# Kernel tuning notes

Hardware: AMD Instinct MI355X
Metric: run time of the kernel (lower is better)

Reference implementation:

```python
import jax, jax.numpy as jnp
import numpy as np

BN_EPS = 1e-5
ITER_N = 5

def _bn(x, gamma, beta, mean, var, axis):
    shape = [1] * x.ndim
    shape[axis] = -1
    r = lambda v: v.reshape(shape)
    return (x - r(mean)) * (r(gamma) / jnp.sqrt(r(var) + BN_EPS)) + r(beta)

def _covpool(x):
    # x: (B, d, M); MPNCOV CovpoolLayer: y = x @ I_hat @ x^T, I_hat = (1/M)I - (1/M^2)11^T
    M = x.shape[-1]
    I_hat = (-1.0 / (M * M)) * jnp.ones((M, M), x.dtype) + (1.0 / M) * jnp.eye(M, dtype=x.dtype)
    return jnp.einsum('bdm,mn,ben->bde', x, I_hat, x)

def _sqrtm_ns(A, iterN=ITER_N):
    # MPNCOV SqrtmLayer: trace-normalized Newton-Schulz iteration
    d = A.shape[-1]
    I3 = 3.0 * jnp.eye(d, dtype=A.dtype)
    normA = jnp.trace(A, axis1=1, axis2=2) / 3.0          # (B,)
    A_n = A / normA[:, None, None]
    ZY = 0.5 * (I3 - A_n)
    Y = A_n @ ZY
    Z = ZY
    for _ in range(iterN - 2):
        ZY = 0.5 * (I3 - Z @ Y)
        Y = Y @ ZY
        Z = ZY @ Z
    YZY = 0.5 * (Y @ (I3 - Z @ Y))
    return YZY * jnp.sqrt(normA)[:, None, None]

def setup_inputs() -> dict:
    key = jax.random.key(0)
    ks = jax.random.split(key, 12)
    B, C, H, W = 64, 1024, 16, 16
    D, R = 128, H * W  # att_dim, sp_reso
    return {
        'x': jax.random.normal(ks[0], (B, C, H, W), jnp.float32),
        'w_dr': jax.random.normal(ks[1], (D, C), jnp.float32) * 0.02,
        'b_dr': jax.random.normal(ks[2], (D,), jnp.float32) * 0.02,
        'bn1_gamma': jnp.ones((D,), jnp.float32),
        'bn1_beta': jnp.zeros((D,), jnp.float32),
        'bn1_mean': jax.random.normal(ks[3], (D,), jnp.float32) * 0.1,
        'bn1_var': jax.random.uniform(ks[4], (D,), jnp.float32, 0.5, 1.5),
        'bn2_gamma': jnp.ones((R,), jnp.float32),
        'bn2_beta': jnp.zeros((R,), jnp.float32),
        'bn2_mean': jax.random.normal(ks[5], (R,), jnp.float32) * 0.1,
        'bn2_var': jax.random.uniform(ks[6], (R,), jnp.float32, 0.5, 1.5),
        'rc_w': jax.random.normal(ks[7], (R,), jnp.float32) * 0.1 + 1.0,
        'rc_b': jax.random.normal(ks[8], (R,), jnp.float32) * 0.02,
        'fc_w': jax.random.normal(ks[9], (R, R * R), jnp.float32) * 0.004,
        'fc_b': jax.random.normal(ks[10], (R,), jnp.float32) * 0.02,
    }

def reference(x, w_dr, b_dr, bn1_gamma, bn1_beta, bn1_mean, bn1_var,
              bn2_gamma, bn2_beta, bn2_mean, bn2_var, rc_w, rc_b, fc_w, fc_b):
    B, C, H, W = x.shape
    # 1x1 dimension-reduction conv + BN + ReLU
    y = jnp.einsum('bchw,dc->bdhw', x, w_dr) + b_dr[None, :, None, None]
    y = jax.nn.relu(_bn(y, bn1_gamma, bn1_beta, bn1_mean, bn1_var, axis=1))
    # (B, D, HW) -> (B, HW, D): HW spatial positions as 'channels', D as samples
    y = y.reshape(B, -1, H * W).transpose(0, 2, 1)
    cov = _covpool(y)                  # (B, HW, HW)
    s = _sqrtm_ns(cov, ITER_N)         # (B, HW, HW)
    # row BN over first HW axis (channels of the (B, HW, HW, 1) view)
    s = _bn(s, bn2_gamma, bn2_beta, bn2_mean, bn2_var, axis=1)
    # grouped (depthwise) 1x1 row conv: per-row scale + bias
    s = s * rc_w[None, :, None] + rc_b[None, :, None]
    att = jax.nn.sigmoid(s.reshape(B, -1) @ fc_w.T + fc_b)   # (B, HW)
    att = att.reshape(B, 1, H, W)
    return x * att
```

## Files before the change

### kernel.cpp

```cpp
#include <hip/hip_runtime.h>

typedef unsigned short u16;
typedef unsigned int   u32;
typedef __attribute__((ext_vector_type(8))) short bf8;
typedef __attribute__((ext_vector_type(4))) float f4;
typedef __attribute__((ext_vector_type(16))) float f16f;

#define MFMA(a,b,c)   __builtin_amdgcn_mfma_f32_16x16x32_bf16(a,b,c,0,0,0)
#define MFMA32(a,b,c) __builtin_amdgcn_mfma_f32_32x32x16_bf16(a,b,c,0,0,0)

__device__ __forceinline__ u16 f2bf(float f){
  u32 u = __float_as_uint(f);
  u += 0x7fffu + ((u >> 16) & 1u);
  return (u16)(u >> 16);
}
__device__ __forceinline__ float bf2f(u16 h){ return __uint_as_float(((u32)h) << 16); }
__device__ __forceinline__ u32 pk2(float a, float b){ return (u32)f2bf(a) | ((u32)f2bf(b) << 16); }

__device__ __forceinline__ void glds16(const u16* g, u16* l){
  __builtin_amdgcn_global_load_lds((const __attribute__((address_space(1))) u32*)g,
                                   (__attribute__((address_space(3))) u32*)l, 16, 0, 0);
}

__device__ __forceinline__ bf8 ldsFrag(const char* m, int row0, int k0, int pitch){
  int l = threadIdx.x & 63;
  int r = row0 + (l & 15);
  int kb = ((k0 + ((l >> 4) << 3)) << 1) ^ ((r & 7) << 4);
  return *(const bf8*)(m + r * pitch + kb);
}
__device__ __forceinline__ void ldsPut(char* m, int row, int col, int pitch, u16 v){
  int kb = (col << 1) ^ ((row & 7) << 4);
  *(u16*)(m + row * pitch + kb) = v;
}

__device__ __forceinline__ bf8 fragNS(const char* m, int r0, int ks, int l){
  int r = r0 + (l & 31);
  int kb = ((ks << 5) + ((l >> 5) << 4)) ^ ((r & 15) << 4);
  return *(const bf8*)(m + r * 256 + kb);
}
__device__ __forceinline__ bf8 fragWT(const char* m, int r0, int ks, int l){
  int r = r0 + (l & 31);
  int kb = ((ks << 5) + ((l >> 5) << 4)) ^ ((r & 15) << 4);
  return *(const bf8*)(m + r * 512 + kb);
}
__device__ __forceinline__ char* nsAddr(char* m, int row, int col4){
  return m + row * 256 + ((col4 << 1) ^ ((row & 15) << 4));
}

__device__ __forceinline__ void mmPass(const char* A, const char* B, f16f (&acc)[2][2],
                                       int R0, int C0, int l){
  #pragma unroll
  for (int ks = 0; ks < 8; ++ks){
    bf8 a0 = fragNS(A, R0,      ks, l);
    bf8 a1 = fragNS(A, R0 + 32, ks, l);
    bf8 b0 = fragNS(B, C0,      ks, l);
    bf8 b1 = fragNS(B, C0 + 32, ks, l);
    acc[0][0] = MFMA32(a0, b0, acc[0][0]); acc[0][1] = MFMA32(a0, b1, acc[0][1]);
    acc[1][0] = MFMA32(a1, b0, acc[1][0]); acc[1][1] = MFMA32(a1, b1, acc[1][1]);
  }
}

__device__ __forceinline__ void writeTile(char* D, const f16f (&acc)[2][2], int R0, int C0, int l,
                                          float scale, float dval, const uint2* adv){
  #pragma unroll
  for (int ri = 0; ri < 2; ++ri)
  #pragma unroll
  for (int ci = 0; ci < 2; ++ci)
  #pragma unroll
  for (int g = 0; g < 4; ++g){
    int srow = C0 + ci * 32 + (l & 31);
    int scol = R0 + ri * 32 + g * 8 + ((l >> 5) << 2);
    float v[4];
    #pragma unroll
    for (int q = 0; q < 4; ++q){
      float x = scale * acc[ri][ci][g * 4 + q];
      x += ((scol + q) == srow) ? dval : 0.f;
      v[q] = x;
    }
    if (adv){
      uint2 ad = adv[(ri * 2 + ci) * 4 + g];
      v[0] += 1.5f * bf2f((u16)ad.x);
      v[1] += 1.5f * bf2f((u16)(ad.x >> 16));
      v[2] += 1.5f * bf2f((u16)ad.y);
      v[3] += 1.5f * bf2f((u16)(ad.y >> 16));
    }
    *(uint2*)nsAddr(D, srow, scol) = make_uint2(pk2(v[0], v[1]), pk2(v[2], v[3]));
  }
}

__global__ __launch_bounds__(256) void k_prep(const float* __restrict__ wdr,
                                              float* __restrict__ logits,
                                              u16* __restrict__ prep){
  int i = blockIdx.x * 256 + threadIdx.x;
  if (i < 16384) logits[i] = 0.f;
  #pragma unroll
  for (int j = 0; j < 2; ++j){
    int e = i + j * 65536;
    int chunk = e >> 13, rem = e & 8191, d = rem >> 6, cb2 = rem & 63;
    int c = ((cb2 * 2) ^ ((d & 7) << 4)) >> 1;
    prep[e] = f2bf(wdr[d * 1024 + chunk * 64 + c]);
  }
}

__global__ __launch_bounds__(512) void k_conv(
    const u16* __restrict__ wprep, const float* __restrict__ x, const float* __restrict__ bdr,
    const float* __restrict__ g1, const float* __restrict__ be1,
    const float* __restrict__ m1, const float* __restrict__ v1,
    u16* __restrict__ Wg, u16* __restrict__ WTg){
  __shared__ union {
    struct { u16 A[2][8192]; u16 Bt[2][2048]; } s;
    struct { float y[128 * 33]; float musum[512]; float mu[32]; } e;
  } sm;
  int t = threadIdx.x;
  int b = blockIdx.x >> 3, hw0 = (blockIdx.x & 7) * 32;
  const float* xb = x + (size_t)b * 262144 + hw0;

  int w = t >> 6, l = t & 63;
  int d0 = (w >> 1) * 32, hh = (w & 1) * 16;
  int lc = l & 15, lr = (l >> 4) * 4;

  const f4 fz = {0.f, 0.f, 0.f, 0.f};
  f4 acc[2]; acc[0] = fz; acc[1] = fz;

  int cp = t >> 5, hwl = t & 31;
  int bo0 = (4 * cp) ^ ((hwl & 7) << 4);
  int bo1 = (4 * cp + 64) ^ ((hwl & 7) << 4);

  glds16(wprep + t * 8,        sm.s.A[0] + t * 8);
  glds16(wprep + 4096 + t * 8, sm.s.A[0] + 4096 + t * 8);
  glds16(wprep + 8192 + t * 8,        sm.s.A[1] + t * 8);
  glds16(wprep + 8192 + 4096 + t * 8, sm.s.A[1] + 4096 + t * 8);
  float br0 = xb[(size_t)(2 * cp)      * 256 + hwl];
  float br1 = xb[(size_t)(2 * cp + 1)  * 256 + hwl];
  float br2 = xb[(size_t)(2 * cp + 32) * 256 + hwl];
  float br3 = xb[(size_t)(2 * cp + 33) * 256 + hwl];

  #pragma unroll
  for (int k = 0; k < 16; ++k){
    if (k >= 1 && k < 15){
      const u16* src = wprep + (k + 1) * 8192;
      glds16(src + t * 8,        sm.s.A[(k + 1) & 1] + t * 8);
      glds16(src + 4096 + t * 8, sm.s.A[(k + 1) & 1] + 4096 + t * 8);
    }
    float nb0 = 0.f, nb1 = 0.f, nb2 = 0.f, nb3 = 0.f;
    if (k < 15){
      int c0 = (k + 1) * 64;
      nb0 = xb[(size_t)(c0 + 2 * cp)      * 256 + hwl];
      nb1 = xb[(size_t)(c0 + 2 * cp + 1)  * 256 + hwl];
      nb2 = xb[(size_t)(c0 + 2 * cp + 32) * 256 + hwl];
      nb3 = xb[(size_t)(c0 + 2 * cp + 33) * 256 + hwl];
    }
    __builtin_amdgcn_sched_barrier(0);
    if (k == 0)       asm volatile("s_waitcnt vmcnt(4)" ::: "memory");
    else if (k == 15) asm volatile("s_waitcnt vmcnt(0)" ::: "memory");
    else              asm volatile("s_waitcnt vmcnt(6)" ::: "memory");
    __builtin_amdgcn_sched_barrier(0);
    *(u32*)((char*)sm.s.Bt[k & 1] + hwl * 128 + bo0) = pk2(br0, br1);
    *(u32*)((char*)sm.s.Bt[k & 1] + hwl * 128 + bo1) = pk2(br2, br3);
    asm volatile("s_waitcnt lgkmcnt(0)" ::: "memory");
    __builtin_amdgcn_sched_barrier(0);
    __builtin_amdgcn_s_barrier();
    __builtin_amdgcn_sched_barrier(0);
    #pragma unroll
    for (int ks = 0; ks < 2; ++ks){
      int k0 = ks * 32;
      bf8 a0 = ldsFrag((const char*)sm.s.A[k & 1], d0,      k0, 128);
      bf8 a1 = ldsFrag((const char*)sm.s.A[k & 1], d0 + 16, k0, 128);
      bf8 b0 = ldsFrag((const char*)sm.s.Bt[k & 1], hh, k0, 128);
      acc[0] = MFMA(a0, b0, acc[0]);
      acc[1] = MFMA(a1, b0, acc[1]);
    }
    __builtin_amdgcn_sched_barrier(0);
    __builtin_amdgcn_s_barrier();
    __builtin_amdgcn_sched_barrier(0);
    br0 = nb0; br1 = nb1; br2 = nb2; br3 = nb3;
  }
  __syncthreads();

  #pragma unroll
  for (int i = 0; i < 2; ++i)
    #pragma unroll
    for (int r = 0; r < 4; ++r){
      int d = d0 + i * 16 + lr + r;
      float s1 = g1[d] * rsqrtf(v1[d] + 1e-5f);
      float t1 = (bdr[d] - m1[d]) * s1 + be1[d];
      int hwp = hh + lc;
      sm.e.y[d * 33 + hwp] = fmaxf(acc[i][r] * s1 + t1, 0.f);
    }
  __syncthreads();
  {
    int part = t >> 5, col = t & 31;
    float s = 0.f;
    #pragma unroll
    for (int i2 = 0; i2 < 8; ++i2) s += sm.e.y[(part * 8 + i2) * 33 + col];
    sm.e.musum[part * 32 + col] = s;
  }
  __syncthreads();
  if (t < 32){
    float m = 0.f;
    #pragma unroll
    for (int p = 0; p < 16; ++p) m += sm.e.musum[p * 32 + t];
    sm.e.mu[t] = m * (1.0f / 128.0f);
  }
  __syncthreads();
  const float ISM = 0.08838834764831845f;
  {
    int hwp = t >> 4, dc = (t & 15) * 8;
    float muv = sm.e.mu[hwp];
    u32 q[4];
    #pragma unroll
    for (int jj = 0; jj < 4; ++jj){
      float a = (sm.e.y[(dc + 2 * jj)     * 33 + hwp] - muv) * ISM;
      float c = (sm.e.y[(dc + 2 * jj + 1) * 33 + hwp] - muv) * ISM;
      q[jj] = pk2(a, c);
    }
    *(uint4*)(Wg + ((size_t)(b * 256 + hw0 + hwp) * 128 + dc)) = make_uint4(q[0], q[1], q[2], q[3]);
  }
  {
    int d = t >> 2, hc = (t & 3) * 8;
    u32 q[4];
    #pragma unroll
    for (int jj = 0; jj < 4; ++jj){
      int h0 = hc + 2 * jj, h1 = hc + 2 * jj + 1;
      float a = (sm.e.y[d * 33 + h0] - sm.e.mu[h0]) * ISM;
      float c = (sm.e.y[d * 33 + h1] - sm.e.mu[h1]) * ISM;
      q[jj] = pk2(a, c);
    }
    *(uint4*)(WTg + ((size_t)(b * 128 + d) * 256 + hw0 + hc)) = make_uint4(q[0], q[1], q[2], q[3]);
  }
}

extern __shared__ char smns[];
__global__ __launch_bounds__(512, 2) void k_ns(const u16* __restrict__ WT,
                                               u16* __restrict__ yf, float* __restrict__ normAg){
  int b = blockIdx.x, t = threadIdx.x;
  char* Yb = smns;
  char* Zb = smns + 32768;
  char* T1 = smns + 65536;
  char* T2 = smns + 98304;
  char* T3 = smns + 131072;
  char* WTl = smns + 65536;
  char* G   = T3;
  float* trp = (float*)smns;

  int w = t >> 6, l = t & 63;
  int wq = w & 3;
  int R0 = (wq >> 1) * 64, C0 = (wq & 1) * 64;

  { const u16* src = WT + (size_t)b * 32768;
    int row = t >> 2, q = t & 3;
    #pragma unroll
    for (int j = 0; j < 8; ++j) {
      int c16 = q + j * 4;
      bf8 v = *(const bf8*)(src + row * 256 + c16 * 8);
      int ph = c16 ^ (row & 15);
      *(bf8*)(WTl + row * 512 + ph * 16) = v;
    }
  }
  if (t == 0) *trp = 0.f;
  __syncthreads();

  int R0g = (w & 3) * 32, C0g = (w >> 2) * 64;
  const f16f fz16 = {};
  f16f gac[2]; gac[0] = fz16; gac[1] = fz16;
  #pragma unroll
  for (int ks = 0; ks < 16; ++ks){
    bf8 a  = fragWT(WTl, R0g,      ks, l);
    bf8 b0 = fragWT(WTl, C0g,      ks, l);
    bf8 b1 = fragWT(WTl, C0g + 32, ks, l);
    gac[0] = MFMA32(a, b0, gac[0]);
    gac[1] = MFMA32(a, b1, gac[1]);
  }
  float tp = 0.f;
  #pragma unroll
  for (int ci = 0; ci < 2; ++ci)
    #pragma unroll
    for (int e = 0; e < 16; ++e){
      int row = R0g + (e & 3) + 8 * (e >> 2) + ((l >> 5) << 2);
      int col = C0g + ci * 32 + (l & 31);
      if (row == col) tp += gac[ci][e];
    }
  #pragma unroll
  for (int off = 32; off > 0; off >>= 1) tp += __shfl_down(tp, off);
  if (l == 0) atomicAdd(trp, tp);
  __syncthreads();

  float normA = fmaxf(*trp / 3.0f, 1e-12f);
  if (t == 0) normAg[b] = normA;
  float inv = 1.0f / normA;
  #pragma unroll
  for (int ci = 0; ci < 2; ++ci)
    #pragma unroll
    for (int g = 0; g < 4; ++g){
      int srow = C0g + ci * 32 + (l & 31);
      int scol = R0g + g * 8 + ((l >> 5) << 2);
      float v0 = gac[ci][g * 4 + 0] * inv, v1 = gac[ci][g * 4 + 1] * inv;
      float v2 = gac[ci][g * 4 + 2] * inv, v3 = gac[ci][g * 4 + 3] * inv;
      *(uint2*)nsAddr(G, srow, scol) = make_uint2(pk2(v0, v1), pk2(v2, v3));
    }
  __syncthreads();

  bf8 gA[8], gB[8];
  #pragma unroll
  for (int ks = 0; ks < 8; ++ks){
    gA[ks] = fragNS(G, C0,      ks, l);
    gB[ks] = fragNS(G, C0 + 32, ks, l);
  }
  { int row = t >> 2, q4 = t & 3;
    #pragma unroll
    for (int j = 0; j < 4; ++j){
      int c16 = q4 * 4 + j;
      int ph = c16 ^ (row & 15);
      bf8 gg = *(const bf8*)(G + row * 256 + ph * 16);
      bf8 yv, zv;
      #pragma unroll
      for (int e = 0; e < 8; ++e){
        int col = c16 * 8 + e;
        float y = -0.5f * bf2f((u16)gg[e]) + ((col == row) ? 1.5f : 0.f);
        yv[e] = (short)f2bf(y);
        zv[e] = (col == row) ? (short)f2bf(-0.5f) : (short)0;
      }
      *(bf8*)(Yb + row * 256 + ph * 16) = yv;
      *(bf8*)(Zb + row * 256 + ph * 16) = zv;
    }
  }
  __syncthreads();

  float z0 = 1.5f;
  for (int it = 0; it < 4; ++it){
    {
      f16f acc[2][2]; acc[0][0] = fz16; acc[0][1] = fz16; acc[1][0] = fz16; acc[1][1] = fz16;
      const char* As = (w < 4) ? Zb : Yb;
      #pragma unroll
      for (int ks = 0; ks < 8; ++ks){
        bf8 a0 = fragNS(As, R0,      ks, l);
        bf8 a1 = fragNS(As, R0 + 32, ks, l);
        acc[0][0] = MFMA32(a0, gA[ks], acc[0][0]); acc[0][1] = MFMA32(a0, gB[ks], acc[0][1]);
        acc[1][0] = MFMA32(a1, gA[ks], acc[1][0]); acc[1][1] = MFMA32(a1, gB[ks], acc[1][1]);
      }
      writeTile((w < 4) ? T1 : T3, acc, R0, C0, l, 1.0f, (w < 4) ? z0 : 0.f, nullptr);
    }
    __syncthreads();

    uint2 adv[16];
    {
      const char* addsrc = (w < 4) ? Zb : Yb;
      #pragma unroll
      for (int ri = 0; ri < 2; ++ri)
      #pragma unroll
      for (int ci = 0; ci < 2; ++ci)
      #pragma unroll
      for (int g = 0; g < 4; ++g){
        int srow = C0 + ci * 32 + (l & 31);
        int scol = R0 + ri * 32 + g * 8 + ((l >> 5) << 2);
        adv[(ri * 2 + ci) * 4 + g] = *(const uint2*)nsAddr((char*)addsrc, srow, scol);
      }
      if (w < 4){
        f16f acc[2][2]; acc[0][0] = fz16; acc[0][1] = fz16; acc[1][0] = fz16; acc[1][1] = fz16;
        mmPass(T1, Yb, acc, R0, C0, l);
        writeTile(T2, acc, R0, C0, l, -0.5f, 0.f, nullptr);
      }
    }
    __syncthreads();

    if ((w >= 4) || (it < 3)){
      f16f acc[2][2]; acc[0][0] = fz16; acc[0][1] = fz16; acc[1][0] = fz16; acc[1][1] = fz16;
      const char* A3 = (w < 4) ? T2 : T3;
      const char* B3 = (w < 4) ? T1 : T2;
      mmPass(A3, B3, acc, R0, C0, l);
      writeTile((w < 4) ? Zb : Yb, acc, R0, C0, l, 1.0f, 0.f, adv);
    }
    __syncthreads();
    z0 *= 1.5f;
  }

  { int row = t >> 2, q = t & 3;
    u16* dst = yf + (size_t)b * 16384 + row * 128;
    #pragma unroll
    for (int j = 0; j < 4; ++j) {
      int c16 = q * 4 + j;
      int ph = c16 ^ (row & 15);
      *(bf8*)(dst + c16 * 8) = *(const bf8*)(Yb + row * 256 + ph * 16);
    }
  }
}

extern __shared__ char smex[];
__global__ __launch_bounds__(512) void k_expand(
    const u16* __restrict__ Wg, const u16* __restrict__ yf, const float* __restrict__ normAg,
    const float* __restrict__ g2, const float* __restrict__ be2, const float* __restrict__ m2,
    const float* __restrict__ v2, const float* __restrict__ rcw, const float* __restrict__ rcb,
    u16* __restrict__ sp){
  int blk = blockIdx.x, b = blk >> 2, iband = blk & 3;
  char* Bm = smex;
  char* Yl = smex + 65536;
  char* El = smex + 98304;
  int t = threadIdx.x;
  { const u16* src = Wg + (size_t)b * 32768;
    int row = t >> 1, q = t & 1;
    #pragma unroll
    for (int j = 0; j < 8; ++j) {
      int c16 = q + j * 2;
      bf8 v = *(const bf8*)(src + row * 128 + c16 * 8);
      int ph = c16 ^ (row & 7);
      *(bf8*)(Bm + row * 256 + ph * 16) = v;
    } }
  { const u16* src = yf + (size_t)b * 16384;
    int row = t >> 2, q = t & 3;
    #pragma unroll
    for (int j = 0; j < 4; ++j) {
      int c16 = q + j * 4;
      bf8 v = *(const bf8*)(src + row * 128 + c16 * 8);
      int ph = c16 ^ (row & 7);
      *(bf8*)(Yl + row * 256 + ph * 16) = v;
    } }
  __syncthreads();
  int w = t >> 6, l = t & 63, lc = l & 15, lr = (l >> 4) * 4;
  const f4 fz = {0.f, 0.f, 0.f, 0.f};
  { int r0 = (w >> 2) * 32, c0 = (w & 3) * 32;
    f4 acc[2][2];
    acc[0][0] = fz; acc[0][1] = fz; acc[1][0] = fz; acc[1][1] = fz;
    #pragma unroll
    for (int kk = 0; kk < 4; ++kk) {
      int k0 = kk * 32;
      bf8 a0 = ldsFrag(Bm, iband * 64 + r0,      k0, 256);
      bf8 a1 = ldsFrag(Bm, iband * 64 + r0 + 16, k0, 256);
      bf8 b0 = ldsFrag(Yl, c0,      k0, 256);
      bf8 b1 = ldsFrag(Yl, c0 + 16, k0, 256);
      acc[0][0] = MFMA(a0, b0, acc[0][0]); acc[0][1] = MFMA(a0, b1, acc[0][1]);
      acc[1][0] = MFMA(a1, b0, acc[1][0]); acc[1][1] = MFMA(a1, b1, acc[1][1]);
    }
    #pragma unroll
    for (int i = 0; i < 2; ++i)
      #pragma unroll
      for (int j = 0; j < 2; ++j)
        #pragma unroll
        for (int r = 0; r < 4; ++r)
          ldsPut(El, r0 + i * 16 + lr + r, c0 + j * 16 + lc, 256, f2bf(acc[i][j][r]));
  }
  __syncthreads();
  { float invs = rsqrtf(normAg[b]);
    int r0 = (w >> 2) * 32, c0 = (w & 3) * 64;
    f4 acc[2][4];
    #pragma unroll
    for (int i = 0; i < 2; ++i)
      #pragma unroll
      for (int j = 0; j < 4; ++j) acc[i][j] = fz;
    #pragma unroll
    for (int kk = 0; kk < 4; ++kk) {
      int k0 = kk * 32;
      bf8 a0 = ldsFrag(El, r0,      k0, 256);
      bf8 a1 = ldsFrag(El, r0 + 16, k0, 256);
      bf8 b0 = ldsFrag(Bm, c0,      k0, 256);
      bf8 b1 = ldsFrag(Bm, c0 + 16, k0, 256);
      bf8 b2 = ldsFrag(Bm, c0 + 32, k0, 256);
      bf8 b3 = ldsFrag(Bm, c0 + 48, k0, 256);
      acc[0][0] = MFMA(a0, b0, acc[0][0]); acc[0][1] = MFMA(a0, b1, acc[0][1]);
      acc[0][2] = MFMA(a0, b2, acc[0][2]); acc[0][3] = MFMA(a0, b3, acc[0][3]);
      acc[1][0] = MFMA(a1, b0, acc[1][0]); acc[1][1] = MFMA(a1, b1, acc[1][1]);
      acc[1][2] = MFMA(a1, b2, acc[1][2]); acc[1][3] = MFMA(a1, b3, acc[1][3]);
    }
    #pragma unroll
    for (int i = 0; i < 2; ++i)
      #pragma unroll
      for (int r = 0; r < 4; ++r) {
        int il = r0 + i * 16 + lr + r;
        int ig = iband * 64 + il;
        float bs = g2[ig] * rsqrtf(v2[ig] + 1e-5f);
        float al = bs * rcw[ig];
        float be = (be2[ig] - m2[ig] * bs) * rcw[ig] + rcb[ig];
        #pragma unroll
        for (int j = 0; j < 4; ++j) {
          int jg = c0 + j * 16 + lc;
          sp[(size_t)b * 65536 + ig * 256 + jg] = f2bf(acc[i][j][r] * invs * al + be);
        }
      }
  }
}

extern __shared__ char smfc[];
__global__ __launch_bounds__(512) void k_fc(const u16* __restrict__ sp,
                                            const float* __restrict__ fcw,
                                            float* __restrict__ logits){
  int kc = blockIdx.x >> 1, rh = blockIdx.x & 1;
  int k0 = kc * 256, rbase = rh * 128;
  char* Al = smfc;
  char* Bl = smfc + 32768;
  int t = threadIdx.x;
  { int row = t >> 3, q = t & 7;
    #pragma unroll
    for (int j = 0; j < 4; ++j) {
      int c16 = q + j * 8;
      bf8 v = *(const bf8*)(sp + (size_t)row * 65536 + k0 + c16 * 8);
      int ph = c16 ^ (row & 7);
      *(bf8*)(Al + row * 512 + ph * 16) = v;
    } }
  { int lane16 = t & 15;
    #pragma unroll
    for (int pass = 0; pass < 4; ++pass) {
      int row = (t >> 4) + pass * 32;
      #pragma unroll
      for (int j = 0; j < 4; ++j) {
        int k = lane16 * 4 + j * 64;
        float4 v = *(const float4*)(fcw + (size_t)(rbase + row) * 65536 + k0 + k);
        int off = (k * 2) ^ ((row & 7) << 4);
        *(u32*)(Bl + row * 512 + off)     = pk2(v.x, v.y);
        *(u32*)(Bl + row * 512 + off + 4) = pk2(v.z, v.w);
      }
    } }
  __syncthreads();
  int w = t >> 6, l = t & 63, lc = l & 15, lr = (l >> 4) * 4;
  int r0 = (w >> 2) * 32, c0 = (w & 3) * 32;
  const f4 fz = {0.f, 0.f, 0.f, 0.f};
  f4 acc[2][2];
  acc[0][0] = fz; acc[0][1] = fz; acc[1][0] = fz; acc[1][1] = fz;
  #pragma unroll
  for (int kk = 0; kk < 8; ++kk) {
    int ks = kk * 32;
    bf8 a0 = ldsFrag(Al, r0,      ks, 512);
    bf8 a1 = ldsFrag(Al, r0 + 16, ks, 512);
    bf8 b0 = ldsFrag(Bl, c0,      ks, 512);
    bf8 b1 = ldsFrag(Bl, c0 + 16, ks, 512);
    acc[0][0] = MFMA(a0, b0, acc[0][0]); acc[0][1] = MFMA(a0, b1, acc[0][1]);
    acc[1][0] = MFMA(a1, b0, acc[1][0]); acc[1][1] = MFMA(a1, b1, acc[1][1]);
  }
  #pragma unroll
  for (int i = 0; i < 2; ++i)
    #pragma unroll
    for (int j = 0; j < 2; ++j)
      #pragma unroll
      for (int r = 0; r < 4; ++r) {
        int row = r0 + i * 16 + lr + r;
        int col = rbase + c0 + j * 16 + lc;
        atomicAdd(logits + row * 256 + col, acc[i][j][r]);
      }
}

__global__ __launch_bounds__(256) void k_mul(const float* __restrict__ x,
                                             const float* __restrict__ logits,
                                             const float* __restrict__ fcb,
                                             float* __restrict__ out, int n4){
  int i = blockIdx.x * 256 + threadIdx.x;
  int str = gridDim.x * 256;
  for (; i < n4; i += str) {
    int e = i << 2;
    int b = e >> 18;
    int hw = e & 255;
    float4 xv = ((const float4*)x)[i];
    float4 lg = *(const float4*)(logits + (b << 8) + hw);
    float4 fb = *(const float4*)(fcb + hw);
    float4 o;
    o.x = xv.x / (1.f + expf(-(lg.x + fb.x)));
    o.y = xv.y / (1.f + expf(-(lg.y + fb.y)));
    o.z = xv.z / (1.f + expf(-(lg.z + fb.z)));
    o.w = xv.w / (1.f + expf(-(lg.w + fb.w)));
    ((float4*)out)[i] = o;
  }
}

extern "C" void kernel_launch(void* const* d_in, const int* in_sizes, int n_in,
                              void* d_out, int out_size, void* d_ws, size_t ws_size,
                              hipStream_t stream){
  const float* x   = (const float*)d_in[0];
  const float* wdr = (const float*)d_in[1];
  const float* bdr = (const float*)d_in[2];
  const float* g1  = (const float*)d_in[3];
  const float* be1 = (const float*)d_in[4];
  const float* m1  = (const float*)d_in[5];
  const float* v1  = (const float*)d_in[6];
  const float* g2  = (const float*)d_in[7];
  const float* be2 = (const float*)d_in[8];
  const float* m2  = (const float*)d_in[9];
  const float* v2  = (const float*)d_in[10];
  const float* rcw = (const float*)d_in[11];
  const float* rcb = (const float*)d_in[12];
  const float* fcw = (const float*)d_in[13];
  const float* fcb = (const float*)d_in[14];
  float* out = (float*)d_out;
  char* ws = (char*)d_ws;
  u16*   Wg  = (u16*)(ws);
  u16*   WTg = (u16*)(ws + (4u  << 20));
  u16*   yfg = (u16*)(ws + (8u  << 20));
  float* nAg = (float*)(ws + (10u << 20));
  u16*   wpr = (u16*)(ws + (10u << 20) + 4096);
  u16*   spg = (u16*)(ws + (11u << 20));
  float* lgt = (float*)(ws + (20u << 20));

  hipFuncSetAttribute((const void*)k_ns,     hipFuncAttributeMaxDynamicSharedMemorySize, 163840);
  hipFuncSetAttribute((const void*)k_expand, hipFuncAttributeMaxDynamicSharedMemorySize, 114688);
  hipFuncSetAttribute((const void*)k_fc,     hipFuncAttributeMaxDynamicSharedMemorySize, 98304);

  k_prep  <<<256,  256, 0,      stream>>>(wdr, lgt, wpr);
  k_conv  <<<512,  512, 0,      stream>>>(wpr, x, bdr, g1, be1, m1, v1, Wg, WTg);
  k_ns    <<<64,   512, 163840, stream>>>(WTg, yfg, nAg);
  k_expand<<<256,  512, 114688, stream>>>(Wg, yfg, nAg, g2, be2, m2, v2, rcw, rcb, spg);
  k_fc    <<<512,  512, 98304,  stream>>>(spg, fcw, lgt);
  k_mul   <<<2048, 256, 0,      stream>>>(x, lgt, fcb, out, 4194304);
}
```

Baseline: 113.7 us.

## Rewrite FC GEMM to load operands directly into registers with split-K partials

The FC kernel no longer stages sp and fc_w tiles through LDS. Each wave now loads its MFMA fragments straight from global memory, and fp32 weights are truncated to bf16 rather than rounded. The atomicAdd accumulation into logits is replaced by per-K-chunk partial buffers, which a new small reduction kernel sums. This removes LDS traffic, barriers and atomic contention, at the cost of an extra launch, an 8 MB partial buffer round-trip, and slightly different weight rounding.

New measurement: 123.8 us. 8.9% more time.

```diff
diff --git a/kernel.cpp b/kernel.cpp
--- a/kernel.cpp
+++ b/kernel.cpp
@@ -188,8 +188,7 @@
       sm.e.y[d * 33 + hwp] = fmaxf(acc[i][r] * s1 + t1, 0.f);
     }
   __syncthreads();
-  {
-    int part = t >> 5, col = t & 31;
+  { int part = t >> 5, col = t & 31;
     float s = 0.f;
     #pragma unroll
     for (int i2 = 0; i2 < 8; ++i2) s += sm.e.y[(part * 8 + i2) * 33 + col];
@@ -204,8 +203,7 @@
   }
   __syncthreads();
   const float ISM = 0.08838834764831845f;
-  {
-    int hwp = t >> 4, dc = (t & 15) * 8;
+  { int hwp = t >> 4, dc = (t & 15) * 8;
     float muv = sm.e.mu[hwp];
     u32 q[4];
     #pragma unroll
@@ -216,8 +214,7 @@
     }
     *(uint4*)(Wg + ((size_t)(b * 256 + hw0 + hwp) * 128 + dc)) = make_uint4(q[0], q[1], q[2], q[3]);
   }
-  {
-    int d = t >> 2, hc = (t & 3) * 8;
+  { int d = t >> 2, hc = (t & 3) * 8;
     u32 q[4];
     #pragma unroll
     for (int jj = 0; jj < 4; ++jj){
@@ -478,62 +475,75 @@
   }
 }
 
-extern __shared__ char smfc[];
-__global__ __launch_bounds__(512) void k_fc(const u16* __restrict__ sp,
+__global__ __launch_bounds__(256) void k_fc(const u16* __restrict__ sp,
                                             const float* __restrict__ fcw,
+                                            float* __restrict__ partial){
+  int kc = blockIdx.x >> 2, rq = blockIdx.x & 3;
+  int t = threadIdx.x, w = t >> 6, l = t & 63;
+  int k0 = kc * 512;
+  int rloc = rq * 64 + w * 16 + (l & 15);
+  int kl = k0 + ((l >> 4) << 3);
+
+  const float* bp  = fcw + (size_t)rloc * 65536 + kl;
+  const u16*  ap0 = sp + (size_t)((l & 15) +  0) * 65536 + kl;
+  const u16*  ap1 = sp + (size_t)((l & 15) + 16) * 65536 + kl;
+  const u16*  ap2 = sp + (size_t)((l & 15) + 32) * 65536 + kl;
+  const u16*  ap3 = sp + (size_t)((l & 15) + 48) * 65536 + kl;
+
+  const f4 fz = {0.f, 0.f, 0.f, 0.f};
+  f4 acc[4]; acc[0] = fz; acc[1] = fz; acc[2] = fz; acc[3] = fz;
+
+  #pragma unroll 4
+  for (int ks = 0; ks < 16; ++ks){
+    float4 f0 = *(const float4*)(bp + ks * 32);
+    float4 f1 = *(const float4*)(bp + ks * 32 + 4);
+    union { u32 u[4]; bf8 v; } bb;
+    bb.u[0] = (__float_as_uint(f0.x) >> 16) | (__float_as_uint(f0.y) & 0xffff0000u);
+    bb.u[1] = (__float_as_uint(f0.z) >> 16) | (__float_as_uint(f0.w) & 0xffff0000u);
+    bb.u[2] = (__float_as_uint(f1.x) >> 16) | (__float_as_uint(f1.y) & 0xffff0000u);
+    bb.u[3] = (__float_as_uint(f1.z) >> 16) | (__float_as_uint(f1.w) & 0xffff0000u);
+    bf8 a0 = *(const bf8*)(ap0 + ks * 32);
+    bf8 a1 = *(const bf8*)(ap1 + ks * 32);
+    bf8 a2 = *(const bf8*)(ap2 + ks * 32);
+    bf8 a3 = *(const bf8*)(ap3 + ks * 32);
+    acc[0] = MFMA(a0, bb.v, acc[0]);
+    acc[1] = MFMA(a1, bb.v, acc[1]);
+    acc[2] = MFMA(a2, bb.v, acc[2]);
+    acc[3] = MFMA(a3, bb.v, acc[3]);
+  }
+
+  float* pout = partial + (size_t)kc * 16384 + rloc;
+  #pragma unroll
+  for (int bt = 0; bt < 4; ++bt)
+    #pragma unroll
+    for (int q = 0; q < 4; ++q){
+      int b = bt * 16 + ((l >> 4) << 2) + q;
+      pout[b * 256] = acc[bt][q];
+    }
+}
+
+__global__ __launch_bounds__(64) void k_red(const float* __restrict__ partial,
                                             float* __restrict__ logits){
-  int kc = blockIdx.x >> 1, rh = blockIdx.x & 1;
-  int k0 = kc * 256, rbase = rh * 128;
-  char* Al = smfc;
-  char* Bl = smfc + 32768;
-  int t = threadIdx.x;
-  { int row = t >> 3, q = t & 7;
-    #pragma unroll
-    for (int j = 0; j < 4; ++j) {
-      int c16 = q + j * 8;
-      bf8 v = *(const bf8*)(sp + (size_t)row * 65536 + k0 + c16 * 8);
-      int ph = c16 ^ (row & 7);
-      *(bf8*)(Al + row * 512 + ph * 16) = v;
-    } }
-  { int lane16 = t & 15;
-    #pragma unroll
-    for (int pass = 0; pass < 4; ++pass) {
-      int row = (t >> 4) + pass * 32;
-      #pragma unroll
-      for (int j = 0; j < 4; ++j) {
-        int k = lane16 * 4 + j * 64;
-        float4 v = *(const float4*)(fcw + (size_t)(rbase + row) * 65536 + k0 + k);
-        int off = (k * 2) ^ ((row & 7) << 4);
-        *(u32*)(Bl + row * 512 + off)     = pk2(v.x, v.y);
-        *(u32*)(Bl + row * 512 + off + 4) = pk2(v.z, v.w);
-      }
-    } }
-  __syncthreads();
-  int w = t >> 6, l = t & 63, lc = l & 15, lr = (l >> 4) * 4;
-  int r0 = (w >> 2) * 32, c0 = (w & 3) * 32;
-  const f4 fz = {0.f, 0.f, 0.f, 0.f};
-  f4 acc[2][2];
-  acc[0][0] = fz; acc[0][1] = fz; acc[1][0] = fz; acc[1][1] = fz;
-  #pragma unroll
-  for (int kk = 0; kk < 8; ++kk) {
-    int ks = kk * 32;
-    bf8 a0 = ldsFrag(Al, r0,      ks, 512);
-    bf8 a1 = ldsFrag(Al, r0 + 16, ks, 512);
-    bf8 b0 = ldsFrag(Bl, c0,      ks, 512);
-    bf8 b1 = ldsFrag(Bl, c0 + 16, ks, 512);
-    acc[0][0] = MFMA(a0, b0, acc[0][0]); acc[0][1] = MFMA(a0, b1, acc[0][1]);
-    acc[1][0] = MFMA(a1, b0, acc[1][0]); acc[1][1] = MFMA(a1, b1, acc[1][1]);
-  }
-  #pragma unroll
-  for (int i = 0; i < 2; ++i)
-    #pragma unroll
-    for (int j = 0; j < 2; ++j)
-      #pragma unroll
-      for (int r = 0; r < 4; ++r) {
-        int row = r0 + i * 16 + lr + r;
-        int col = rbase + c0 + j * 16 + lc;
-        atomicAdd(logits + row * 256 + col, acc[i][j][r]);
-      }
+  int i4 = blockIdx.x * 64 + threadIdx.x;
+  const float4* p4 = (const float4*)partial;
+  float4 s0 = {0,0,0,0}, s1 = {0,0,0,0}, s2 = {0,0,0,0}, s3 = {0,0,0,0};
+  #pragma unroll 8
+  for (int kc = 0; kc < 128; kc += 4){
+    float4 a = p4[(size_t)(kc + 0) * 4096 + i4];
+    float4 b = p4[(size_t)(kc + 1) * 4096 + i4];
+    float4 c = p4[(size_t)(kc + 2) * 4096 + i4];
+    float4 d = p4[(size_t)(kc + 3) * 4096 + i4];
+    s0.x += a.x; s0.y += a.y; s0.z += a.z; s0.w += a.w;
+    s1.x += b.x; s1.y += b.y; s1.z += b.z; s1.w += b.w;
+    s2.x += c.x; s2.y += c.y; s2.z += c.z; s2.w += c.w;
+    s3.x += d.x; s3.y += d.y; s3.z += d.z; s3.w += d.w;
+  }
+  float4 s;
+  s.x = (s0.x + s1.x) + (s2.x + s3.x);
+  s.y = (s0.y + s1.y) + (s2.y + s3.y);
+  s.z = (s0.z + s1.z) + (s2.z + s3.z);
+  s.w = (s0.w + s1.w) + (s2.w + s3.w);
+  ((float4*)logits)[i4] = s;
 }
 
 __global__ __launch_bounds__(256) void k_mul(const float* __restrict__ x,
@@ -585,15 +595,16 @@
   u16*   wpr = (u16*)(ws + (10u << 20) + 4096);
   u16*   spg = (u16*)(ws + (11u << 20));
   float* lgt = (float*)(ws + (20u << 20));
+  float* prt = (float*)(ws + (24u << 20));
 
   hipFuncSetAttribute((const void*)k_ns,     hipFuncAttributeMaxDynamicSharedMemorySize, 163840);
   hipFuncSetAttribute((const void*)k_expand, hipFuncAttributeMaxDynamicSharedMemorySize, 114688);
-  hipFuncSetAttribute((const void*)k_fc,     hipFuncAttributeMaxDynamicSharedMemorySize, 98304);
 
   k_prep  <<<256,  256, 0,      stream>>>(wdr, lgt, wpr);
   k_conv  <<<512,  512, 0,      stream>>>(wpr, x, bdr, g1, be1, m1, v1, Wg, WTg);
   k_ns    <<<64,   512, 163840, stream>>>(WTg, yfg, nAg);
   k_expand<<<256,  512, 114688, stream>>>(Wg, yfg, nAg, g2, be2, m2, v2, rcw, rcb, spg);
-  k_fc    <<<512,  512, 98304,  stream>>>(spg, fcw, lgt);
+  k_fc    <<<512,  256, 0,      stream>>>(spg, fcw, prt);
+  k_red   <<<64,   64,  0,      stream>>>(prt, lgt);
   k_mul   <<<2048, 256, 0,      stream>>>(x, lgt, fcb, out, 4194304);
 }
```
